# Performance work log

Measured on AMD Instinct MI355X. Metric: run time of the kernel, lower is better.

## Reference

```python
import jax, jax.numpy as jnp
import numpy as np

H = 768
NH = 12
HD = H // NH  # 64


def setup_inputs() -> dict:
    key = jax.random.key(0)
    ks = jax.random.split(key, 12)
    B, SQ, SK = 8, 1024, 1024
    s = 1.0 / np.sqrt(H)
    return {
        "hidden_states": jax.random.normal(ks[0], (B, SQ, H), jnp.float32),
        "condition_embeddings": jax.random.normal(ks[1], (B, SK, H), jnp.float32),
        "condition_mask": jnp.ones((B, SK), jnp.float32),
        "Wq": jax.random.normal(ks[2], (H, H), jnp.float32) * s,
        "bq": jnp.zeros((H,), jnp.float32),
        "Wk": jax.random.normal(ks[3], (H, H), jnp.float32) * s,
        "bk": jnp.zeros((H,), jnp.float32),
        "Wv": jax.random.normal(ks[4], (H, H), jnp.float32) * s,
        "bv": jnp.zeros((H,), jnp.float32),
        "Wo": jax.random.normal(ks[5], (H, H), jnp.float32) * s,
        "bo": jnp.zeros((H,), jnp.float32),
        "ln_g": jnp.ones((H,), jnp.float32),
        "ln_b": jnp.zeros((H,), jnp.float32),
    }


def _heads(x):
    # [B, S, H] -> [B, NH, S, HD]
    B, S, _ = x.shape
    return x.reshape(B, S, NH, HD).transpose(0, 2, 1, 3)


def reference(hidden_states, condition_embeddings, condition_mask,
              Wq, bq, Wk, bk, Wv, bv, Wo, bo, ln_g, ln_b):
    q = _heads(hidden_states @ Wq.T + bq)            # [B,NH,SQ,HD]
    k = _heads(condition_embeddings @ Wk.T + bk)     # [B,NH,SK,HD]
    v = _heads(condition_embeddings @ Wv.T + bv)     # [B,NH,SK,HD]

    scores = jnp.einsum("bhqd,bhkd->bhqk", q, k) / np.sqrt(HD)
    ext_mask = (1.0 - condition_mask)[:, None, None, :] * -10000.0
    scores = scores + ext_mask
    probs = jax.nn.softmax(scores, axis=-1)          # dropout = identity (eval)

    ctx = jnp.einsum("bhqk,bhkd->bhqd", probs, v)    # [B,NH,SQ,HD]
    B, _, SQ, _ = ctx.shape
    ctx = ctx.transpose(0, 2, 1, 3).reshape(B, SQ, H)

    out = ctx @ Wo.T + bo
    x = hidden_states + out
    mu = jnp.mean(x, axis=-1, keepdims=True)
    var = jnp.var(x, axis=-1, keepdims=True)
    return (x - mu) / jnp.sqrt(var + 1e-5) * ln_g + ln_b
```

## Files before the change

### kernel.cpp

```cpp
#include <hip/hip_runtime.h>
#include <stdint.h>

#define B_ 8
#define S_ 1024
#define H_ 768
#define NH_ 12
#define HD_ 64
#define M_ (B_*S_)

typedef __attribute__((ext_vector_type(8))) short short8;
typedef __attribute__((ext_vector_type(8))) ushort ushort8;
typedef __attribute__((ext_vector_type(4))) float floatx4;

#define MFMA16(a,b,c) __builtin_amdgcn_mfma_f32_16x16x32_bf16((a),(b),(c),0,0,0)

__device__ __forceinline__ ushort f2bf(float x){
    union { float f; unsigned u; } v; v.f = x;
    unsigned r = (v.u + 0x7fffu + ((v.u >> 16) & 1u)) >> 16;
    return (ushort)r;
}

__device__ __forceinline__ void async16(const ushort* g, ushort* l){
    __builtin_amdgcn_global_load_lds(
        (const __attribute__((address_space(1))) unsigned int*)g,
        (__attribute__((address_space(3))) unsigned int*)l, 16, 0, 0);
}

__global__ __launch_bounds__(256, 8) void cvt_all(
    const float* __restrict__ hs, const float* __restrict__ ce,
    const float* __restrict__ wq, const float* __restrict__ wk,
    const float* __restrict__ wv, const float* __restrict__ wo,
    ushort* __restrict__ hsb, ushort* __restrict__ ceb,
    ushort* __restrict__ wqb, ushort* __restrict__ wkb,
    ushort* __restrict__ wvb, ushort* __restrict__ wob)
{
    const int NA = M_*H_/8;
    const int NW = H_*H_/8;
    int i = blockIdx.x*256 + threadIdx.x;
    if (i >= 2*NA + 4*NW) return;
    const float* s; ushort* d; int off;
    if (i < NA)            { s = hs; d = hsb; off = i; }
    else if (i < 2*NA)     { s = ce; d = ceb; off = i - NA; }
    else {
        int j = i - 2*NA;
        int wsel = j / NW;
        off = j - wsel*NW;
        s = (wsel==0) ? wq : (wsel==1) ? wk : (wsel==2) ? wv : wo;
        d = (wsel==0) ? wqb : (wsel==1) ? wkb : (wsel==2) ? wvb : wob;
    }
    float4 f0 = ((const float4*)s)[2*off];
    float4 f1 = ((const float4*)s)[2*off + 1];
    ushort8 u;
    u[0] = f2bf(f0.x); u[1] = f2bf(f0.y); u[2] = f2bf(f0.z); u[3] = f2bf(f0.w);
    u[4] = f2bf(f1.x); u[5] = f2bf(f1.y); u[6] = f2bf(f1.z); u[7] = f2bf(f1.w);
    ((ushort8*)d)[off] = u;
}

template<int BN, int MODE>
__device__ __forceinline__ void gemm_body(
    ushort* __restrict__ smem,
    const ushort* __restrict__ A, const ushort* __restrict__ Bw,
    const float* __restrict__ bias, ushort* __restrict__ obf,
    float* __restrict__ of32, const float* __restrict__ resid,
    int bx, int by)
{
    constexpr int NT = BN/32;
    ushort* lA = smem;
    ushort* lB = smem + 8192;
    const int K = H_;
    int tid  = threadIdx.x;
    int lane = tid & 63, wave = tid >> 6;
    int m0 = bx * 128, n0 = by * BN;
    int wm = (wave >> 1) * 64, wn = (wave & 1) * (BN/2);
    int fr = lane & 15, quad = lane >> 4, quad4 = quad*4;

    floatx4 acc[4][NT];
    #pragma unroll
    for (int mt=0;mt<4;mt++)
        #pragma unroll
        for (int nt=0;nt<NT;nt++)
            acc[mt][nt] = (floatx4){0.f,0.f,0.f,0.f};

    int row0 = tid >> 3;
    int csw  = ((tid & 7) ^ (row0 & 7)) * 8;
    const ushort* Ap[4]; const ushort* Bp[NT];
    ushort* ldA_[4]; ushort* ldB_[NT];
    #pragma unroll
    for (int j=0;j<4;j++){
        int row = row0 + 32*j;
        Ap[j] = A + (size_t)(m0 + row) * K + csw;
        ldA_[j] = lA + (tid + 256*j)*8;
    }
    #pragma unroll
    for (int j=0;j<NT;j++){
        int row = row0 + 32*j;
        Bp[j] = Bw + (size_t)(n0 + row) * K + csw;
        ldB_[j] = lB + (tid + 256*j)*8;
    }

    for (int k0 = 0; k0 < K; k0 += 64){
        #pragma unroll
        for (int j=0;j<4;j++) async16(Ap[j] + k0, ldA_[j]);
        #pragma unroll
        for (int j=0;j<NT;j++) async16(Bp[j] + k0, ldB_[j]);
        __syncthreads();
        #pragma unroll
        for (int kk=0; kk<2; kk++){
            short8 af[4], bfr[NT];
            #pragma unroll
            for (int t=0;t<4;t++){
                int ra = wm + t*16 + fr;
                af[t]  = *(const short8*)&lA[ra*64 + (((kk*4+quad) ^ (ra&7))<<3)];
            }
            #pragma unroll
            for (int t=0;t<NT;t++){
                int rb = wn + t*16 + fr;
                bfr[t] = *(const short8*)&lB[rb*64 + (((kk*4+quad) ^ (rb&7))<<3)];
            }
            #pragma unroll
            for (int mt=0;mt<4;mt++)
                #pragma unroll
                for (int nt=0;nt<NT;nt++)
                    acc[mt][nt] = MFMA16(af[mt], bfr[nt], acc[mt][nt]);
        }
        __syncthreads();
    }

    float bv_[NT];
    #pragma unroll
    for (int nt=0;nt<NT;nt++) bv_[nt] = bias[n0 + wn + nt*16 + fr];

    if constexpr (MODE == 0){
        #pragma unroll
        for (int mt=0;mt<4;mt++){
            int rb = m0 + wm + mt*16 + quad4;
            #pragma unroll
            for (int nt=0;nt<NT;nt++){
                int col = n0 + wn + nt*16 + fr;
                #pragma unroll
                for (int r=0;r<4;r++)
                    obf[(size_t)(rb + r)*H_ + col] = f2bf(acc[mt][nt][r] + bv_[nt]);
            }
        }
    } else if constexpr (MODE == 1){
        int bb = m0 >> 10, q0 = m0 & 1023;
        #pragma unroll
        for (int mt=0;mt<4;mt++){
            int ql = wm + mt*16 + quad4;
            #pragma unroll
            for (int nt=0;nt<NT;nt++){
                int dl = wn + nt*16 + fr;
                ushort4 u;
                u.x = f2bf(acc[mt][nt][0] + bv_[nt]);
                u.y = f2bf(acc[mt][nt][1] + bv_[nt]);
                u.z = f2bf(acc[mt][nt][2] + bv_[nt]);
                u.w = f2bf(acc[mt][nt][3] + bv_[nt]);
                *(ushort4*)&smem[dl*136 + ql] = u;
            }
        }
        __syncthreads();
        #pragma unroll
        for (int jj=0;jj<6;jj++){
            int mI = tid + 256*jj;
            int d  = mI >> 4;
            int qc = (mI & 15) * 8;
            short8 v = *(const short8*)&smem[d*136 + qc];
            int gcol = by*96 + d;
            int h = gcol >> 6, dd = gcol & 63;
            *(short8*)&obf[((size_t)((bb*NH_ + h)*HD_ + dd))*S_ + q0 + qc] = v;
        }
    } else {
        #pragma unroll
        for (int mt=0;mt<4;mt++){
            int rb = m0 + wm + mt*16 + quad4;
            #pragma unroll
            for (int nt=0;nt<NT;nt++){
                int col = n0 + wn + nt*16 + fr;
                #pragma unroll
                for (int r=0;r<4;r++){
                    size_t idx = (size_t)(rb + r)*H_ + col;
                    of32[idx] = acc[mt][nt][r] + bv_[nt] + resid[idx];
                }
            }
        }
    }
}

__global__ __launch_bounds__(256, 3) void gemm_qkv(
    const ushort* __restrict__ hsb, const ushort* __restrict__ ceb,
    const ushort* __restrict__ wqb, const ushort* __restrict__ wkb,
    const ushort* __restrict__ wvb,
    const float* __restrict__ bq, const float* __restrict__ bk,
    const float* __restrict__ bv,
    ushort* __restrict__ Qb, ushort* __restrict__ Kb, ushort* __restrict__ Vtb)
{
    __shared__ ushort smem[8192 + 96*64];
    int z = blockIdx.z;
    const ushort* A  = (z==0) ? hsb : ceb;
    const ushort* Bw = (z==0) ? wqb : (z==1) ? wkb : wvb;
    const float* bias = (z==0) ? bq : (z==1) ? bk : bv;
    if (z == 2)
        gemm_body<96,1>(smem, A, Bw, bias, Vtb, nullptr, nullptr,
                        blockIdx.x, blockIdx.y);
    else
        gemm_body<96,0>(smem, A, Bw, bias, (z==0)?Qb:Kb, nullptr, nullptr,
                        blockIdx.x, blockIdx.y);
}

__global__ __launch_bounds__(256, 3) void gemm_o(
    const ushort* __restrict__ ctxb, const ushort* __restrict__ wob,
    const float* __restrict__ bo, const float* __restrict__ hs,
    float* __restrict__ proj)
{
    __shared__ ushort smem[8192 + 96*64];
    gemm_body<96,2>(smem, ctxb, wob, bo, nullptr, proj, hs,
                    blockIdx.x, blockIdx.y);
}

__global__ __launch_bounds__(256, 3) void attn(
    const ushort* __restrict__ Q, const ushort* __restrict__ Kc,
    const ushort* __restrict__ Vt, const float* __restrict__ mask,
    ushort* __restrict__ ctx)
{
    __shared__ ushort lK[64*64];
    __shared__ ushort lV[64*64];
    __shared__ ushort lP[4][32*72];
    __shared__ float  lmask[S_];
    __shared__ float  linv[4][32];

    const float SC = 0.125f * 1.44269504f;

    int bid = blockIdx.x;
    int qt = bid & 7;
    int h  = (bid >> 3) % NH_;
    int b  = bid / (8*NH_);

    int tid  = threadIdx.x;
    int lane = tid & 63, w = tid >> 6;
    int fr = lane & 15, quad = lane >> 4;
    int quad4 = quad*4, sw = fr & 7;

    for (int i = tid; i < S_; i += 256)
        lmask[i] = (1.0f - mask[b*S_ + i]) * -14426.95f;

    short8 qf[2][2];
    #pragma unroll
    for (int nq=0;nq<2;nq++){
        const ushort* Qp = Q + (size_t)(b*S_ + qt*128 + w*32 + nq*16 + fr)*H_ + h*HD_ + quad*8;
        qf[nq][0] = *(const short8*)(Qp);
        qf[nq][1] = *(const short8*)(Qp + 32);
    }

    floatx4 O[2][4];
    #pragma unroll
    for (int mt=0;mt<2;mt++)
        #pragma unroll
        for (int nt=0;nt<4;nt++)
            O[mt][nt] = (floatx4){0.f,0.f,0.f,0.f};
    float rs0 = 0.f, rs1 = 0.f;

    int n0 = tid,       r0 = n0 >> 3, c0 = (n0 & 7) ^ (r0 & 7);
    int n1 = 256 + tid, r1 = n1 >> 3, c1 = (n1 & 7) ^ (r1 & 7);
    const ushort* pK0 = Kc + (size_t)(b*S_ + r0)*H_ + h*HD_ + c0*8;
    const ushort* pK1 = Kc + (size_t)(b*S_ + r1)*H_ + h*HD_ + c1*8;
    const ushort* pV0 = Vt + ((size_t)(b*NH_ + h)*HD_ + r0)*S_ + c0*8;
    const ushort* pV1 = Vt + ((size_t)(b*NH_ + h)*HD_ + r1)*S_ + c1*8;
    ushort* dK0 = &lK[n0*8]; ushort* dK1 = &lK[n1*8];
    ushort* dV0 = &lV[n0*8]; ushort* dV1 = &lV[n1*8];

    ushort* lPw = &lP[w][0];

    for (int kt = 0; kt < 16; kt++){
        __syncthreads();
        async16(pK0, dK0); async16(pK1, dK1);
        async16(pV0, dV0); async16(pV1, dV1);
        pK0 += (size_t)64*H_; pK1 += (size_t)64*H_;
        pV0 += 64; pV1 += 64;
        __syncthreads();

        float4 mk4[4];
        #pragma unroll
        for (int mk=0;mk<4;mk++)
            mk4[mk] = *(const float4*)&lmask[kt*64 + mk*16 + quad4];

        short8 kf[4][2];
        #pragma unroll
        for (int mk=0;mk<4;mk++){
            int row = mk*16 + fr;
            kf[mk][0] = *(const short8*)&lK[row*64 + ((quad     ^ sw)<<3)];
            kf[mk][1] = *(const short8*)&lK[row*64 + (((4+quad) ^ sw)<<3)];
        }
        __builtin_amdgcn_s_setprio(1);
        floatx4 st[2][4];
        #pragma unroll
        for (int nq=0;nq<2;nq++)
            #pragma unroll
            for (int mk=0;mk<4;mk++){
                floatx4 a = (floatx4){0.f,0.f,0.f,0.f};
                a = MFMA16(kf[mk][0], qf[nq][0], a);
                a = MFMA16(kf[mk][1], qf[nq][1], a);
                st[nq][mk] = a;
            }
        __builtin_amdgcn_s_setprio(0);

        #pragma unroll
        for (int nq=0;nq<2;nq++){
            #pragma unroll
            for (int mk=0;mk<4;mk++){
                floatx4 s = st[nq][mk];
                #pragma unroll
                for (int r=0;r<4;r++)
                    s[r] = __builtin_amdgcn_exp2f(s[r]*SC + mk4[mk][r]);
                if (nq == 0) rs0 += (s[0]+s[1]) + (s[2]+s[3]);
                else         rs1 += (s[0]+s[1]) + (s[2]+s[3]);
                unsigned lo = __builtin_amdgcn_perm(__float_as_uint(s[1]), __float_as_uint(s[0]), 0x07060302u);
                unsigned hi = __builtin_amdgcn_perm(__float_as_uint(s[3]), __float_as_uint(s[2]), 0x07060302u);
                uint2 pk; pk.x = lo; pk.y = hi;
                *(uint2*)&lPw[(nq*16 + fr)*72 + mk*16 + quad4] = pk;
            }
        }

        short8 vf[4][2];
        #pragma unroll
        for (int nt=0;nt<4;nt++){
            int row = nt*16 + fr;
            vf[nt][0] = *(const short8*)&lV[row*64 + ((quad     ^ sw)<<3)];
            vf[nt][1] = *(const short8*)&lV[row*64 + (((4+quad) ^ sw)<<3)];
        }
        short8 pf[2][2];
        #pragma unroll
        for (int mt=0;mt<2;mt++){
            pf[mt][0] = *(const short8*)&lPw[(mt*16+fr)*72 + quad*8];
            pf[mt][1] = *(const short8*)&lPw[(mt*16+fr)*72 + 32 + quad*8];
        }
        __builtin_amdgcn_s_setprio(1);
        #pragma unroll
        for (int mt=0;mt<2;mt++)
            #pragma unroll
            for (int nt=0;nt<4;nt++){
                O[mt][nt] = MFMA16(pf[mt][0], vf[nt][0], O[mt][nt]);
                O[mt][nt] = MFMA16(pf[mt][1], vf[nt][1], O[mt][nt]);
            }
        __builtin_amdgcn_s_setprio(0);
    }

    rs0 += __shfl_xor(rs0, 16); rs0 += __shfl_xor(rs0, 32);
    rs1 += __shfl_xor(rs1, 16); rs1 += __shfl_xor(rs1, 32);
    if (lane < 16){
        linv[w][fr]      = 1.0f / rs0;
        linv[w][16 + fr] = 1.0f / rs1;
    }
    int tokbase = b*S_ + qt*128 + w*32;
    #pragma unroll
    for (int mt=0;mt<2;mt++){
        float4 iv = *(const float4*)&linv[w][mt*16 + quad4];
        #pragma unroll
        for (int nt=0;nt<4;nt++)
            #pragma unroll
            for (int r=0;r<4;r++){
                int tok = tokbase + mt*16 + quad4 + r;
                ctx[(size_t)tok*H_ + h*HD_ + nt*16 + fr] = f2bf(O[mt][nt][r] * (&iv.x)[r]);
            }
    }
}

__global__ __launch_bounds__(192, 4) void resid_ln(
    const float* __restrict__ x,
    const float* __restrict__ g, const float* __restrict__ be,
    float* __restrict__ out)
{
    int row = blockIdx.x;
    int tid = threadIdx.x;
    float4 v = ((const float4*)(x + (size_t)row*H_))[tid];
    float s  = (v.x + v.y) + (v.z + v.w);
    float s2 = (v.x*v.x + v.y*v.y) + (v.z*v.z + v.w*v.w);
    #pragma unroll
    for (int off=1; off<64; off<<=1){
        s  += __shfl_xor(s,  off);
        s2 += __shfl_xor(s2, off);
    }
    __shared__ float rs[3], rs2[3];
    if ((tid & 63) == 0){ rs[tid>>6] = s; rs2[tid>>6] = s2; }
    __syncthreads();
    s  = rs[0]+rs[1]+rs[2];
    s2 = rs2[0]+rs2[1]+rs2[2];
    float mu  = s * (1.f/H_);
    float var = s2*(1.f/H_) - mu*mu;
    float rinv = rsqrtf(var + 1e-5f);
    float4 gg = ((const float4*)g)[tid];
    float4 bb = ((const float4*)be)[tid];
    float4 o;
    o.x = (v.x-mu)*rinv*gg.x + bb.x;
    o.y = (v.y-mu)*rinv*gg.y + bb.y;
    o.z = (v.z-mu)*rinv*gg.z + bb.z;
    o.w = (v.w-mu)*rinv*gg.w + bb.w;
    ((float4*)(out + (size_t)row*H_))[tid] = o;
}

extern "C" void kernel_launch(void* const* d_in, const int* in_sizes, int n_in,
                              void* d_out, int out_size, void* d_ws, size_t ws_size,
                              hipStream_t stream)
{
    (void)in_sizes; (void)n_in; (void)out_size; (void)ws_size;
    const float* hs   = (const float*)d_in[0];
    const float* ce   = (const float*)d_in[1];
    const float* mask = (const float*)d_in[2];
    const float* Wq   = (const float*)d_in[3];
    const float* bq   = (const float*)d_in[4];
    const float* Wk   = (const float*)d_in[5];
    const float* bk   = (const float*)d_in[6];
    const float* Wv   = (const float*)d_in[7];
    const float* bv   = (const float*)d_in[8];
    const float* Wo   = (const float*)d_in[9];
    const float* bo   = (const float*)d_in[10];
    const float* lg   = (const float*)d_in[11];
    const float* lb   = (const float*)d_in[12];
    float* out = (float*)d_out;

    char* ws = (char*)d_ws;
    const size_t SZ_ACT = (size_t)M_*H_*2;
    const size_t SZ_W   = (size_t)H_*H_*2;
    ushort* hsb  = (ushort*)(ws);
    ushort* ceb  = (ushort*)(ws + SZ_ACT);
    ushort* wqb  = (ushort*)(ws + 2*SZ_ACT);
    ushort* wkb  = (ushort*)(ws + 2*SZ_ACT + 1*SZ_W);
    ushort* wvb  = (ushort*)(ws + 2*SZ_ACT + 2*SZ_W);
    ushort* wob  = (ushort*)(ws + 2*SZ_ACT + 3*SZ_W);
    ushort* Qb   = (ushort*)(ws + 2*SZ_ACT + 4*SZ_W);
    ushort* Kb   = (ushort*)(ws + 3*SZ_ACT + 4*SZ_W);
    ushort* Vtb  = (ushort*)(ws + 4*SZ_ACT + 4*SZ_W);
    ushort* ctxb = (ushort*)(ws + 5*SZ_ACT + 4*SZ_W);
    float*  proj = (float*)(ws);

    int ncvt = 2*(M_*H_/8) + 4*(H_*H_/8);
    cvt_all<<<dim3((ncvt+255)/256), dim3(256), 0, stream>>>(
        hs, ce, Wq, Wk, Wv, Wo, hsb, ceb, wqb, wkb, wvb, wob);

    gemm_qkv<<<dim3(M_/128, H_/96, 3), dim3(256), 0, stream>>>(
        hsb, ceb, wqb, wkb, wvb, bq, bk, bv, Qb, Kb, Vtb);

    attn<<<dim3(B_*NH_*8), dim3(256), 0, stream>>>(Qb, Kb, Vtb, mask, ctxb);

    gemm_o<<<dim3(M_/128, H_/96), dim3(256), 0, stream>>>(ctxb, wob, bo, hs, proj);

    resid_ln<<<dim3(M_), dim3(192), 0, stream>>>(proj, lg, lb, out);
}
```

Before: 222.5 us.

## Fuse output projection and LayerNorm via cooperative grid sync

Merges the output-projection GEMM and the residual LayerNorm into one cooperative kernel. After the GEMM tiles are written, a grid-wide barrier is taken and each block then normalizes 16 rows, one wavefront per row. This removes one kernel launch and the separate LN pass's launch gap. In exchange it adds a grid-wide sync, and the kernel depends on all 512 blocks being co-resident for the cooperative launch to succeed.

```diff
diff --git a/kernel.cpp b/kernel.cpp
--- a/kernel.cpp
+++ b/kernel.cpp
@@ -1,5 +1,8 @@
 #include <hip/hip_runtime.h>
+#include <hip/hip_cooperative_groups.h>
 #include <stdint.h>
+
+namespace cg = cooperative_groups;
 
 #define B_ 8
 #define S_ 1024
@@ -207,14 +210,61 @@
                         blockIdx.x, blockIdx.y);
 }
 
-__global__ __launch_bounds__(256, 3) void gemm_o(
+__global__ __launch_bounds__(256, 3) void gemm_o_ln(
     const ushort* __restrict__ ctxb, const ushort* __restrict__ wob,
     const float* __restrict__ bo, const float* __restrict__ hs,
-    float* __restrict__ proj)
+    float* __restrict__ proj,
+    const float* __restrict__ g, const float* __restrict__ be,
+    float* __restrict__ out)
 {
     __shared__ ushort smem[8192 + 96*64];
     gemm_body<96,2>(smem, ctxb, wob, bo, nullptr, proj, hs,
                     blockIdx.x, blockIdx.y);
+
+    __threadfence();
+    cg::this_grid().sync();
+
+    int tid  = threadIdx.x;
+    int lane = tid & 63, w4 = tid >> 6;
+    int lin  = blockIdx.y * gridDim.x + blockIdx.x;
+    #pragma unroll
+    for (int it = 0; it < 4; ++it){
+        int row = lin*16 + it*4 + w4;
+        const float* pr = proj + (size_t)row * H_;
+        float4 v0 = ((const float4*)pr)[lane];
+        float4 v1 = ((const float4*)pr)[lane + 64];
+        float4 v2 = ((const float4*)pr)[lane + 128];
+        float s  = (v0.x+v0.y+v0.z+v0.w) + (v1.x+v1.y+v1.z+v1.w)
+                 + (v2.x+v2.y+v2.z+v2.w);
+        float s2 = (v0.x*v0.x+v0.y*v0.y+v0.z*v0.z+v0.w*v0.w)
+                 + (v1.x*v1.x+v1.y*v1.y+v1.z*v1.z+v1.w*v1.w)
+                 + (v2.x*v2.x+v2.y*v2.y+v2.z*v2.z+v2.w*v2.w);
+        #pragma unroll
+        for (int off=1; off<64; off<<=1){
+            s  += __shfl_xor(s,  off);
+            s2 += __shfl_xor(s2, off);
+        }
+        float mu  = s * (1.f/H_);
+        float var = s2*(1.f/H_) - mu*mu;
+        float rinv = rsqrtf(var + 1e-5f);
+        float4 g0 = ((const float4*)g)[lane];
+        float4 g1 = ((const float4*)g)[lane + 64];
+        float4 g2 = ((const float4*)g)[lane + 128];
+        float4 b0 = ((const float4*)be)[lane];
+        float4 b1 = ((const float4*)be)[lane + 64];
+        float4 b2 = ((const float4*)be)[lane + 128];
+        float* po = out + (size_t)row * H_;
+        float4 o0, o1, o2;
+        o0.x=(v0.x-mu)*rinv*g0.x+b0.x; o0.y=(v0.y-mu)*rinv*g0.y+b0.y;
+        o0.z=(v0.z-mu)*rinv*g0.z+b0.z; o0.w=(v0.w-mu)*rinv*g0.w+b0.w;
+        o1.x=(v1.x-mu)*rinv*g1.x+b1.x; o1.y=(v1.y-mu)*rinv*g1.y+b1.y;
+        o1.z=(v1.z-mu)*rinv*g1.z+b1.z; o1.w=(v1.w-mu)*rinv*g1.w+b1.w;
+        o2.x=(v2.x-mu)*rinv*g2.x+b2.x; o2.y=(v2.y-mu)*rinv*g2.y+b2.y;
+        o2.z=(v2.z-mu)*rinv*g2.z+b2.z; o2.w=(v2.w-mu)*rinv*g2.w+b2.w;
+        ((float4*)po)[lane]       = o0;
+        ((float4*)po)[lane + 64]  = o1;
+        ((float4*)po)[lane + 128] = o2;
+    }
 }
 
 __global__ __launch_bounds__(256, 3) void attn(
@@ -362,39 +412,6 @@
                 ctx[(size_t)tok*H_ + h*HD_ + nt*16 + fr] = f2bf(O[mt][nt][r] * (&iv.x)[r]);
             }
     }
-}
-
-__global__ __launch_bounds__(192, 4) void resid_ln(
-    const float* __restrict__ x,
-    const float* __restrict__ g, const float* __restrict__ be,
-    float* __restrict__ out)
-{
-    int row = blockIdx.x;
-    int tid = threadIdx.x;
-    float4 v = ((const float4*)(x + (size_t)row*H_))[tid];
-    float s  = (v.x + v.y) + (v.z + v.w);
-    float s2 = (v.x*v.x + v.y*v.y) + (v.z*v.z + v.w*v.w);
-    #pragma unroll
-    for (int off=1; off<64; off<<=1){
-        s  += __shfl_xor(s,  off);
-        s2 += __shfl_xor(s2, off);
-    }
-    __shared__ float rs[3], rs2[3];
-    if ((tid & 63) == 0){ rs[tid>>6] = s; rs2[tid>>6] = s2; }
-    __syncthreads();
-    s  = rs[0]+rs[1]+rs[2];
-    s2 = rs2[0]+rs2[1]+rs2[2];
-    float mu  = s * (1.f/H_);
-    float var = s2*(1.f/H_) - mu*mu;
-    float rinv = rsqrtf(var + 1e-5f);
-    float4 gg = ((const float4*)g)[tid];
-    float4 bb = ((const float4*)be)[tid];
-    float4 o;
-    o.x = (v.x-mu)*rinv*gg.x + bb.x;
-    o.y = (v.y-mu)*rinv*gg.y + bb.y;
-    o.z = (v.z-mu)*rinv*gg.z + bb.z;
-    o.w = (v.w-mu)*rinv*gg.w + bb.w;
-    ((float4*)(out + (size_t)row*H_))[tid] = o;
 }
 
 extern "C" void kernel_launch(void* const* d_in, const int* in_sizes, int n_in,
@@ -441,7 +458,9 @@
 
     attn<<<dim3(B_*NH_*8), dim3(256), 0, stream>>>(Qb, Kb, Vtb, mask, ctxb);
 
-    gemm_o<<<dim3(M_/128, H_/96), dim3(256), 0, stream>>>(ctxb, wob, bo, hs, proj);
-
-    resid_ln<<<dim3(M_), dim3(192), 0, stream>>>(proj, lg, lb, out);
-}
+    void* args[] = { (void*)&ctxb, (void*)&wob, (void*)&bo, (void*)&hs,
+                     (void*)&proj, (void*)&lg, (void*)&lb, (void*)&out };
+    hipLaunchCooperativeKernel((const void*)gemm_o_ln,
+                               dim3(M_/128, H_/96), dim3(256),
+                               args, 0, stream);
+}
```

Result: slower. 359.6 us (+61.6%).

## Fuse K and V projections into one GEMM block sharing the A tile

Applied to the files above, without the earlier changes.

Adds a combined K/V GEMM body in which each block loads the condition-embedding tile once and multiplies it against both the Wk and Wv tiles, producing K and transposed V. The QKV launch drops from three z-slices to two, which removes a redundant read of the condition activations. In exchange the KV blocks hold twice the accumulators and use more shared memory (20480 shorts), which may reduce occupancy. The grid also becomes imbalanced, since the KV blocks do double the work of the Q blocks.

```diff
diff --git a/kernel.cpp b/kernel.cpp
--- a/kernel.cpp
+++ b/kernel.cpp
@@ -186,6 +186,133 @@
     }
 }
 
+__device__ __forceinline__ void gemm_kv_body(
+    ushort* __restrict__ smem,
+    const ushort* __restrict__ A,
+    const ushort* __restrict__ Bk, const ushort* __restrict__ Bv,
+    const float* __restrict__ biask, const float* __restrict__ biasv,
+    ushort* __restrict__ Kb, ushort* __restrict__ Vtb,
+    int bx, int by)
+{
+    ushort* lA  = smem;
+    ushort* lBK = smem + 8192;
+    ushort* lBV = smem + 14336;
+    const int K = H_;
+    int tid  = threadIdx.x;
+    int lane = tid & 63, wave = tid >> 6;
+    int m0 = bx * 128, n0 = by * 96;
+    int wm = (wave >> 1) * 64, wn = (wave & 1) * 48;
+    int fr = lane & 15, quad = lane >> 4, quad4 = quad*4;
+
+    floatx4 aK[4][3], aV[4][3];
+    #pragma unroll
+    for (int mt=0;mt<4;mt++)
+        #pragma unroll
+        for (int nt=0;nt<3;nt++){
+            aK[mt][nt] = (floatx4){0.f,0.f,0.f,0.f};
+            aV[mt][nt] = (floatx4){0.f,0.f,0.f,0.f};
+        }
+
+    int row0 = tid >> 3;
+    int csw  = ((tid & 7) ^ (row0 & 7)) * 8;
+    const ushort* Ap[4]; const ushort* Kp[3]; const ushort* Vp[3];
+    ushort* ldA_[4]; ushort* ldK_[3]; ushort* ldV_[3];
+    #pragma unroll
+    for (int j=0;j<4;j++){
+        int row = row0 + 32*j;
+        Ap[j] = A + (size_t)(m0 + row) * K + csw;
+        ldA_[j] = lA + (tid + 256*j)*8;
+    }
+    #pragma unroll
+    for (int j=0;j<3;j++){
+        int row = row0 + 32*j;
+        Kp[j] = Bk + (size_t)(n0 + row) * K + csw;
+        Vp[j] = Bv + (size_t)(n0 + row) * K + csw;
+        ldK_[j] = lBK + (tid + 256*j)*8;
+        ldV_[j] = lBV + (tid + 256*j)*8;
+    }
+
+    for (int k0 = 0; k0 < K; k0 += 64){
+        #pragma unroll
+        for (int j=0;j<4;j++) async16(Ap[j] + k0, ldA_[j]);
+        #pragma unroll
+        for (int j=0;j<3;j++) async16(Kp[j] + k0, ldK_[j]);
+        #pragma unroll
+        for (int j=0;j<3;j++) async16(Vp[j] + k0, ldV_[j]);
+        __syncthreads();
+        #pragma unroll
+        for (int kk=0; kk<2; kk++){
+            short8 af[4], bk_[3], bv2_[3];
+            #pragma unroll
+            for (int t=0;t<4;t++){
+                int ra = wm + t*16 + fr;
+                af[t] = *(const short8*)&lA[ra*64 + (((kk*4+quad) ^ (ra&7))<<3)];
+            }
+            #pragma unroll
+            for (int t=0;t<3;t++){
+                int rb = wn + t*16 + fr;
+                int off = (((kk*4+quad) ^ (rb&7))<<3);
+                bk_[t]  = *(const short8*)&lBK[rb*64 + off];
+                bv2_[t] = *(const short8*)&lBV[rb*64 + off];
+            }
+            #pragma unroll
+            for (int mt=0;mt<4;mt++)
+                #pragma unroll
+                for (int nt=0;nt<3;nt++){
+                    aK[mt][nt] = MFMA16(af[mt], bk_[nt],  aK[mt][nt]);
+                    aV[mt][nt] = MFMA16(af[mt], bv2_[nt], aV[mt][nt]);
+                }
+        }
+        __syncthreads();
+    }
+
+    float bk4[3], bv4[3];
+    #pragma unroll
+    for (int nt=0;nt<3;nt++){
+        bk4[nt] = biask[n0 + wn + nt*16 + fr];
+        bv4[nt] = biasv[n0 + wn + nt*16 + fr];
+    }
+
+    #pragma unroll
+    for (int mt=0;mt<4;mt++){
+        int rb = m0 + wm + mt*16 + quad4;
+        #pragma unroll
+        for (int nt=0;nt<3;nt++){
+            int col = n0 + wn + nt*16 + fr;
+            #pragma unroll
+            for (int r=0;r<4;r++)
+                Kb[(size_t)(rb + r)*H_ + col] = f2bf(aK[mt][nt][r] + bk4[nt]);
+        }
+    }
+
+    int bb = m0 >> 10, q0 = m0 & 1023;
+    #pragma unroll
+    for (int mt=0;mt<4;mt++){
+        int ql = wm + mt*16 + quad4;
+        #pragma unroll
+        for (int nt=0;nt<3;nt++){
+            int dl = wn + nt*16 + fr;
+            ushort4 u;
+            u.x = f2bf(aV[mt][nt][0] + bv4[nt]);
+            u.y = f2bf(aV[mt][nt][1] + bv4[nt]);
+            u.z = f2bf(aV[mt][nt][2] + bv4[nt]);
+            u.w = f2bf(aV[mt][nt][3] + bv4[nt]);
+            *(ushort4*)&smem[dl*136 + ql] = u;
+        }
+    }
+    __syncthreads();
+    #pragma unroll
+    for (int jj=0;jj<6;jj++){
+        int mI = tid + 256*jj;
+        int d  = mI >> 4;
+        int qc = (mI & 15) * 8;
+        short8 v = *(const short8*)&smem[d*136 + qc];
+        int gcol = by*96 + d;
+        int h = gcol >> 6, dd = gcol & 63;
+        *(short8*)&Vtb[((size_t)((bb*NH_ + h)*HD_ + dd))*S_ + q0 + qc] = v;
+    }
+}
+
 __global__ __launch_bounds__(256, 3) void gemm_qkv(
     const ushort* __restrict__ hsb, const ushort* __restrict__ ceb,
     const ushort* __restrict__ wqb, const ushort* __restrict__ wkb,
@@ -194,17 +321,13 @@
     const float* __restrict__ bv,
     ushort* __restrict__ Qb, ushort* __restrict__ Kb, ushort* __restrict__ Vtb)
 {
-    __shared__ ushort smem[8192 + 96*64];
-    int z = blockIdx.z;
-    const ushort* A  = (z==0) ? hsb : ceb;
-    const ushort* Bw = (z==0) ? wqb : (z==1) ? wkb : wvb;
-    const float* bias = (z==0) ? bq : (z==1) ? bk : bv;
-    if (z == 2)
-        gemm_body<96,1>(smem, A, Bw, bias, Vtb, nullptr, nullptr,
+    __shared__ ushort smem[20480];
+    if (blockIdx.z == 0)
+        gemm_body<96,0>(smem, hsb, wqb, bq, Qb, nullptr, nullptr,
                         blockIdx.x, blockIdx.y);
     else
-        gemm_body<96,0>(smem, A, Bw, bias, (z==0)?Qb:Kb, nullptr, nullptr,
-                        blockIdx.x, blockIdx.y);
+        gemm_kv_body(smem, ceb, wkb, wvb, bk, bv, Kb, Vtb,
+                     blockIdx.x, blockIdx.y);
 }
 
 __global__ __launch_bounds__(256, 3) void gemm_o(
@@ -436,7 +559,7 @@
     cvt_all<<<dim3((ncvt+255)/256), dim3(256), 0, stream>>>(
         hs, ce, Wq, Wk, Wv, Wo, hsb, ceb, wqb, wkb, wvb, wob);
 
-    gemm_qkv<<<dim3(M_/128, H_/96, 3), dim3(256), 0, stream>>>(
+    gemm_qkv<<<dim3(M_/128, H_/96, 2), dim3(256), 0, stream>>>(
         hsb, ceb, wqb, wkb, wvb, bq, bk, bv, Qb, Kb, Vtb);
 
     attn<<<dim3(B_*NH_*8), dim3(256), 0, stream>>>(Qb, Kb, Vtb, mask, ctxb);
```

New measurement: 221.9 us. No clear change (-0.3%).
